# Performance work log

Measured on AMD Instinct MI355X. Metric: run time of the kernel, lower is better.

## Reference

```python
import jax, jax.numpy as jnp
import numpy as np
from jax.scipy.special import logsumexp

B, N, K = 4, 2048, 20          # batch, points per cloud, knn neighbors
D_EMB, H = 512, 4              # embedding dim, attention heads
DH = D_EMB // H                # per-head dim (128)


def setup_inputs() -> dict:
    key = jax.random.key(0)
    ks = jax.random.split(key, 24)
    rn = lambda i, shape, s=0.05: jax.random.normal(ks[i], shape, jnp.float32) * s
    sc = lambda i, c: 1.0 + 0.1 * jax.random.normal(ks[i], (c,), jnp.float32)  # folded BN scale
    return {
        "src": jax.random.normal(ks[0], (B, 3, N), jnp.float32),
        "tgt": jax.random.normal(ks[1], (B, 3, N), jnp.float32),
        # GACLayer (shared for src/tgt): conv(6->64), conv(64->128), out conv(192->512); BN folded to scale/bias
        "g_w1": rn(2, (64, 6)),   "g_s1": sc(3, 64),  "g_b1": rn(4, (64,), 0.02),
        "g_w2": rn(5, (128, 64)), "g_s2": sc(6, 128), "g_b2": rn(7, (128,), 0.02),
        "g_wo": rn(8, (D_EMB, 192)), "g_so": sc(9, D_EMB), "g_bo": rn(10, (D_EMB,), 0.02),
        # MultiHeadedAttention: 3 projection 1x1 convs + merge (all with bias), mlp 1024->512 no bias
        "q_w": rn(11, (D_EMB, D_EMB)), "q_b": rn(12, (D_EMB,), 0.02),
        "k_w": rn(13, (D_EMB, D_EMB)), "k_b": rn(14, (D_EMB,), 0.02),
        "v_w": rn(15, (D_EMB, D_EMB)), "v_b": rn(16, (D_EMB,), 0.02),
        "m_w": rn(17, (D_EMB, D_EMB)), "m_b": rn(18, (D_EMB,), 0.02),
        "mlp_w": rn(19, (D_EMB, 2 * D_EMB)),
    }


def _forward(src, tgt, g_w1, g_s1, g_b1, g_w2, g_s2, g_b2, g_wo, g_so, g_bo,
             q_w, q_b, k_w, k_b, v_w, v_b, m_w, m_b, mlp_w):
    def knn_idx(x):                     # x: [B,3,N] -> [B,N,K] nearest-neighbor indices
        xx = jnp.sum(x * x, axis=1)                      # [B,N]
        inner = jnp.einsum('bdn,bdm->bnm', x, x)
        neg_d = 2.0 * inner - xx[:, :, None] - xx[:, None, :]   # negative sq dist
        return jax.lax.top_k(neg_d, K)[1]                # same as sort-descending[:k]

    def graph_feature(x):               # x: [B,D,N] -> [B,2D,N,K]
        idx = knn_idx(x)
        xt = x.transpose(0, 2, 1)                        # [B,N,D]
        feat = xt[jnp.arange(B)[:, None, None], idx]     # gather: [B,N,K,D]
        ctr = jnp.broadcast_to(xt[:, :, None, :], feat.shape)
        g = jnp.concatenate([feat - ctr, ctr], axis=-1)  # [B,N,K,2D]
        return g.transpose(0, 3, 1, 2)

    def conv_bn_relu2d(w, s, b, x):     # 1x1 conv2d + folded BN (eval) + relu
        y = jnp.einsum('oc,bcnk->bonk', w, x)
        return jax.nn.relu(y * s[:, None, None] + b[:, None, None])

    def attn_pool(h):                   # softmax over neighbors, weighted sum
        a = jax.nn.softmax(h, axis=-1)
        return jnp.sum(h * a, axis=-1)

    def gac(x):                         # GACLayer: [B,3,N] -> [B,512,N]
        g = graph_feature(x)            # [B,6,N,K]
        h1 = conv_bn_relu2d(g_w1, g_s1, g_b1, g)
        x1 = attn_pool(h1)              # [B,64,N]
        h2 = conv_bn_relu2d(g_w2, g_s2, g_b2, h1)
        x2 = attn_pool(h2)              # [B,128,N]
        o = jnp.einsum('oc,bcn->bon', g_wo, jnp.concatenate([x1, x2], axis=1))
        return jax.nn.relu(o * g_so[:, None] + g_bo[:, None])

    def proj(w, b, x):                  # 1x1 conv1d with bias
        return jnp.einsum('oi,bin->bon', w, x) + b[:, None]

    def mha(x, source):                 # note torch view splits channels as (dim, heads)
        q = proj(q_w, q_b, x).reshape(B, DH, H, -1)
        k_ = proj(k_w, k_b, source).reshape(B, DH, H, -1)
        v_ = proj(v_w, v_b, source).reshape(B, DH, H, -1)
        scores = jnp.einsum('bdhn,bdhm->bhnm', q, k_) / jnp.sqrt(jnp.float32(DH))
        prob = jax.nn.softmax(scores, axis=-1)
        msg = jnp.einsum('bhnm,bdhm->bdhn', prob, v_)
        return proj(m_w, m_b, msg.reshape(B, D_EMB, -1))

    def prop(x, source):                # AttentionalPropagation (mlp: 1024->512, no bias/relu)
        msg = mha(x, source)
        return jnp.einsum('oi,bin->bon', mlp_w, jnp.concatenate([x, msg], axis=1))

    def sinkhorn(scores, n_iters=5):    # log-domain Sinkhorn with dustbin row/col (zero pad)
        s = jnp.pad(scores, ((0, 0), (0, 1), (0, 1)))
        for _ in range(n_iters):
            s = jnp.concatenate(
                [s[:, :-1, :] - logsumexp(s[:, :-1, :], axis=2, keepdims=True), s[:, -1:, :]], axis=1)
            s = jnp.concatenate(
                [s[:, :, :-1] - logsumexp(s[:, :, :-1], axis=1, keepdims=True), s[:, :, -1:]], axis=2)
        return s[:, :-1, :-1]

    # embed + cross attentional GNN (shared layer, residual)
    d0, d1 = gac(src), gac(tgt)
    d0, d1 = d0 + prop(d0, d1), d1 + prop(d1, d0)

    dists = jnp.einsum('bdn,bdm->bnm', d0, d1) / jnp.sqrt(jnp.float32(D_EMB))
    perm = jnp.exp(sinkhorn(dists))
    perm_norm = perm / (jnp.sum(perm, axis=2, keepdims=True) + 1e-8)

    weighted_tgt = jnp.einsum('bdm,bnm->bdn', tgt, perm_norm)        # [B,3,N]
    weights = jnp.max(perm, axis=-1, keepdims=True)                  # [B,N,1]
    w_norm = (weights / (jnp.sum(weights, axis=1, keepdims=True) + 1e-8)).transpose(0, 2, 1)  # [B,1,N]
    src_c = jnp.sum(src * w_norm, axis=2, keepdims=True)             # [B,3,1]
    tgt_c = jnp.sum(weighted_tgt * w_norm, axis=2, keepdims=True)
    src_cent = src - src_c
    corr_cent = (weighted_tgt - tgt_c) * w_norm
    Hm = jnp.einsum('bdn,ben->bde', src_cent, corr_cent)             # [B,3,3]

    def solve(Hi):                      # Kabsch with reflection fix (torch.svd returns V, not V^T)
        u, s_, vt = jnp.linalg.svd(Hi)
        v = vt.T
        det = jnp.linalg.det(v @ u.T)
        diag = jnp.diag(jnp.concatenate([jnp.ones(2, Hi.dtype), det[None]]))
        return v @ diag @ u.T

    R = jax.vmap(solve)(Hm)
    t = (-jnp.einsum('bij,bjk->bik', R, src_c) + tgt_c).reshape(B, 3)
    return R, t, perm_norm


def reference(src, tgt, g_w1, g_s1, g_b1, g_w2, g_s2, g_b2, g_wo, g_so, g_bo,
              q_w, q_b, k_w, k_b, v_w, v_b, m_w, m_b, mlp_w):
    return _forward(src, tgt, g_w1, g_s1, g_b1, g_w2, g_s2, g_b2, g_wo, g_so, g_bo,
                    q_w, q_b, k_w, k_b, v_w, v_b, m_w, m_b, mlp_w)
```

## Files before the change

### kernel.cpp

```cpp
#include <hip/hip_runtime.h>
#include <math.h>

#define BATCH 4
#define NP    2048
#define KNNK  20
#define DEMB  512
#define NH    4
#define DHD   128

typedef __attribute__((ext_vector_type(8))) short bf16x8;
typedef __attribute__((ext_vector_type(4))) float f32x4;

__device__ __forceinline__ unsigned short f2b(float f) {
  unsigned u = __builtin_bit_cast(unsigned, f);
  u += 0x7FFF + ((u >> 16) & 1);
  return (unsigned short)(u >> 16);
}
__device__ __forceinline__ float b2f(unsigned short u) {
  unsigned v = ((unsigned)u) << 16;
  return __builtin_bit_cast(float, v);
}

__device__ __forceinline__ void gload_lds16(const void* g, void* l) {
  __builtin_amdgcn_global_load_lds(
// ... 124 lines not shown
    h1f[p][k][o] = y;
    h1b[p * 2048 + k * 64 + (((o >> 3) ^ (k & 7)) << 3) + (o & 7)] = f2b(y);
  }
  __syncthreads();

  {
    int p = w, o = lane;
    float mx = -INFINITY;
#pragma unroll
    for (int k = 0; k < 20; ++k) mx = fmaxf(mx, h1f[p][k][o]);
    float se = 0.f, sh = 0.f;
#pragma unroll
    for (int k = 0; k < 20; ++k) {
      float h = h1f[p][k][o];
      float e = __expf(h - mx);
      se += e; sh += h * e;
    }
    xcg[(size_t)(pbase + p) * 192 + o] = f2b(sh / se);
  }

  bf16x8 bfrag[2][2];
#pragma unroll
  for (int ks = 0; ks < 2; ++ks)
#pragma unroll
    for (int nt = 0; nt < 2; ++nt) {
      int kcol = nt * 16 + lr;
      int oc = ks * 4 + lg;
      bfrag[ks][nt] = *(const bf16x8*)&h1b[w * 2048 + kcol * 64 + ((oc ^ (kcol & 7)) << 3)];
    }
  f32x4 acc[8][2];
#pragma unroll
  for (int i = 0; i < 8; ++i) { acc[i][0] = (f32x4){0,0,0,0}; acc[i][1] = (f32x4){0,0,0,0}; }
#pragma unroll
  for (int i = 0; i < 8; ++i)
#pragma unroll
    for (int ks = 0; ks < 2; ++ks) {
      bf16x8 a = *(const bf16x8*)(w2b + (i * 16 + lr) * 64 + ks * 32 + lg * 8);
      acc[i][0] = __builtin_amdgcn_mfma_f32_16x16x32_bf16(a, bfrag[ks][0], acc[i][0], 0, 0, 0);
      acc[i][1] = __builtin_amdgcn_mfma_f32_16x16x32_bf16(a, bfrag[ks][1], acc[i][1], 0, 0, 0);
    }
  int pt = pbase + w;
#pragma unroll
  for (int i = 0; i < 8; ++i) {
    float x2o[4];
#pragma unroll
    for (int r = 0; r < 4; ++r) {
      int o = i * 16 + lg * 4 + r;
      float sv = s2[o], bv = b2[o];
      float v0 = fmaxf(acc[i][0][r] * sv + bv, 0.f);
      float v1 = fmaxf(acc[i][1][r] * sv + bv, 0.f);
      float vm = (lr < 4) ? fmaxf(v0, v1) : v0;
#pragma unroll
      for (int s = 1; s < 16; s <<= 1) vm = fmaxf(vm, __shfl_xor(vm, s));
      float e0 = __expf(v0 - vm);
      float e1 = (lr < 4) ? __expf(v1 - vm) : 0.f;
      float se = e0 + e1, sh = v0 * e0 + v1 * e1;
#pragma unroll
      for (int s = 1; s < 16; s <<= 1) { se += __shfl_xor(se, s); sh += __shfl_xor(sh, s); }
      x2o[r] = sh / se;
    }
    if (lr == 0) {
      ushort4 pk;
      pk.x = f2b(x2o[0]); pk.y = f2b(x2o[1]); pk.z = f2b(x2o[2]); pk.w = f2b(x2o[3]);
      *(ushort4*)&xcg[(size_t)pt * 192 + 64 + i * 16 + lg * 4] = pk;
    }
  }
}

__global__ __launch_bounds__(256, 2) void gacproj_kernel(
    const unsigned short* __restrict__ wob, const float* __restrict__ so,
    const float* __restrict__ bo, const unsigned short* __restrict__ xcg,
    unsigned short* __restrict__ Y0, unsigned short* __restrict__ Y1) {
  __shared__ __align__(16) unsigned short Al[128 * 64];
  __shared__ __align__(16) unsigned short Bl[128 * 64];
  int n0 = blockIdx.x * 128, o0 = blockIdx.y * 128;
  unsigned short* Yt = (n0 < BATCH * NP) ? Y0 : Y1;
  int nbase = n0 & (BATCH * NP - 1);
  int tid = threadIdx.x, w = tid >> 6, lane = tid & 63;
  int lr = lane & 15, lg = lane >> 4;
  int wa = w >> 1, wb = w & 1;
  f32x4 acc[4][4];
#pragma unroll
  for (int i = 0; i < 4; ++i)
#pragma unroll
    for (int j = 0; j < 4; ++j) acc[i][j] = (f32x4){0.f, 0.f, 0.f, 0.f};

  for (int k0 = 0; k0 < 192; k0 += 64) {
    __syncthreads();
#pragma unroll
    for (int u = 0; u < 4; ++u) {
      int C = u * 256 + tid;
      int row = C >> 3, j = C & 7;
      int js = j ^ (row & 7);
      gload_lds16(wob + (size_t)(o0 + row) * 192 + k0 + js * 8, Al + (u * 256 + w * 64) * 8);
      gload_lds16(xcg + (size_t)(n0 + row) * 192 + k0 + js * 8, Bl + (u * 256 + w * 64) * 8);
    }
    asm volatile("s_waitcnt vmcnt(0)" ::: "memory");
    __syncthreads();
#pragma unroll
    for (int kk = 0; kk < 2; ++kk) {
      bf16x8 af[4], bfr[4];
#pragma unroll
      for (int i = 0; i < 4; ++i) {
        int rowa = wa * 64 + i * 16 + lr;
        int ca = (kk * 4 + lg) ^ (rowa & 7);
        af[i] = *(const bf16x8*)(Al + rowa * 64 + ca * 8);
        int rowb = wb * 64 + i * 16 + lr;
        int cb = (kk * 4 + lg) ^ (rowb & 7);
        bfr[i] = *(const bf16x8*)(Bl + rowb * 64 + cb * 8);
      }
#pragma unroll
      for (int i = 0; i < 4; ++i)
#pragma unroll
        for (int j = 0; j < 4; ++j)
          acc[i][j] = __builtin_amdgcn_mfma_f32_16x16x32_bf16(af[i], bfr[j], acc[i][j], 0, 0, 0);
    }
  }
#pragma unroll
  for (int i = 0; i < 4; ++i) {
#pragma unroll
    for (int j = 0; j < 4; ++j) {
      int obase = o0 + wa * 64 + i * 16 + lg * 4;
      int n = nbase + wb * 64 + j * 16 + lr;
      ushort4 pk;
      pk.x = f2b(fmaxf(acc[i][j][0] * so[obase] + bo[obase], 0.f));
      pk.y = f2b(fmaxf(acc[i][j][1] * so[obase + 1] + bo[obase + 1], 0.f));
      pk.z = f2b(fmaxf(acc[i][j][2] * so[obase + 2] + bo[obase + 2], 0.f));
      pk.w = f2b(fmaxf(acc[i][j][3] * so[obase + 3] + bo[obase + 3], 0.f));
      *(ushort4*)&Yt[(size_t)n * DEMB + obase] = pk;
    }
  }
}

__global__ __launch_bounds__(256, 2) void qkv_kernel(
    const unsigned short* __restrict__ qw, const unsigned short* __restrict__ kw,
    const unsigned short* __restrict__ vw, const float* __restrict__ qbias,
    const float* __restrict__ kbias, const float* __restrict__ vbias,
    const unsigned short* __restrict__ d0t, const unsigned short* __restrict__ d1t,
    unsigned short* __restrict__ Q0, unsigned short* __restrict__ K0,
    unsigned short* __restrict__ V0, unsigned short* __restrict__ Q1,
    unsigned short* __restrict__ K1, unsigned short* __restrict__ V1) {
  __shared__ __align__(16) unsigned short Al[128 * 64];
  __shared__ __align__(16) unsigned short Bl[128 * 64];
  int z = blockIdx.z;
  int b = z & 3, which = z >> 2;
  int proj = which % 3, side = which / 3;
  const unsigned short* Wb = (proj == 0) ? qw : (proj == 1) ? kw : vw;
  const float* bias = (proj == 0) ? qbias : (proj == 1) ? kbias : vbias;
  const unsigned short* Bt = side ? d1t : d0t;
  unsigned short* Y = (which == 0) ? Q0 : (which == 1) ? K0 : (which == 2) ? V0
                    : (which == 3) ? Q1 : (which == 4) ? K1 : V1;
  float pscale = (proj == 0) ? 0.08838834764831845f : 1.f;
  int n0 = blockIdx.x * 128, o0 = blockIdx.y * 128;
  int tid = threadIdx.x, w = tid >> 6, lane = tid & 63;
  int lr = lane & 15, lg = lane >> 4;
  int wa = w >> 1, wb = w & 1;
  f32x4 acc[4][4];
#pragma unroll
  for (int i = 0; i < 4; ++i)
#pragma unroll
    for (int j = 0; j < 4; ++j) acc[i][j] = (f32x4){0.f, 0.f, 0.f, 0.f};

  for (int k0 = 0; k0 < DEMB; k0 += 64) {
    __syncthreads();
#pragma unroll
    for (int u = 0; u < 4; ++u) {
      int C = u * 256 + tid;
      int row = C >> 3, j = C & 7;
      int js = j ^ (row & 7);
      gload_lds16(Wb + (size_t)(o0 + row) * DEMB + k0 + js * 8, Al + (u * 256 + w * 64) * 8);
      gload_lds16(Bt + ((size_t)b * NP + n0 + row) * 512 + k0 + js * 8,
                  Bl + (u * 256 + w * 64) * 8);
    }
    asm volatile("s_waitcnt vmcnt(0)" ::: "memory");
    __syncthreads();
#pragma unroll
    for (int kk = 0; kk < 2; ++kk) {
      bf16x8 af[4], bfr[4];
#pragma unroll
      for (int i = 0; i < 4; ++i) {
        int rowa = wa * 64 + i * 16 + lr;
        int ca = (kk * 4 + lg) ^ (rowa & 7);
        af[i] = *(const bf16x8*)(Al + rowa * 64 + ca * 8);
        int rowb = wb * 64 + i * 16 + lr;
        int cb = (kk * 4 + lg) ^ (rowb & 7);
        bfr[i] = *(const bf16x8*)(Bl + rowb * 64 + cb * 8);
      }
#pragma unroll
      for (int i = 0; i < 4; ++i)
#pragma unroll
        for (int j = 0; j < 4; ++j)
          acc[i][j] = __builtin_amdgcn_mfma_f32_16x16x32_bf16(af[i], bfr[j], acc[i][j], 0, 0, 0);
    }
  }
#pragma unroll
  for (int i = 0; i < 4; ++i) {
#pragma unroll
    for (int j = 0; j < 4; ++j) {
#pragma unroll
      for (int r = 0; r < 4; ++r) {
        int o = o0 + wa * 64 + i * 16 + lg * 4 + r;
        int n = n0 + wb * 64 + j * 16 + lr;
        float v = (acc[i][j][r] + bias[o]) * pscale;
        int h = o & 3, dh = o >> 2;
        if (proj < 2) {
          Y[(((size_t)b * NH + h) * NP + n) * DHD + dh] = f2b(v);
        } else {
          Y[(((size_t)b * NH + h) * DHD + dh) * NP + n] = f2b(v);
        }
      }
    }
  }
}

template <int MODE, int KD>
__global__ __launch_bounds__(256, 2) void proj_mfma_kernel(
    const unsigned short* __restrict__ Wb, const float* __restrict__ bias,
    const unsigned short* __restrict__ Bt0, const unsigned short* __restrict__ Bt1,
    const unsigned short* __restrict__ Bt2_0, const unsigned short* __restrict__ Bt2_1,
    const unsigned short* __restrict__ D0, const unsigned short* __restrict__ D1,
    unsigned short* __restrict__ Y0, unsigned short* __restrict__ Y1) {
  __shared__ __align__(16) unsigned short Al[128 * 64];
  __shared__ __align__(16) unsigned short Bl[128 * 64];
  int z = blockIdx.z;
  int b = z & 3, side = z >> 2;
  const unsigned short* Bt = side ? Bt1 : Bt0;
  const unsigned short* Bt2 = side ? Bt2_1 : Bt2_0;
  const unsigned short* Dres = side ? D1 : D0;
  unsigned short* Y = side ? Y1 : Y0;
  int n0 = blockIdx.x * 128, o0 = blockIdx.y * 128;
  int tid = threadIdx.x, w = tid >> 6, lane = tid & 63;
  int lr = lane & 15, lg = lane >> 4;
  int wa = w >> 1, wb = w & 1;
  f32x4 acc[4][4];
#pragma unroll
  for (int i = 0; i < 4; ++i)
#pragma unroll
    for (int j = 0; j < 4; ++j) acc[i][j] = (f32x4){0.f, 0.f, 0.f, 0.f};

  for (int k0 = 0; k0 < KD; k0 += 64) {
    __syncthreads();
    const unsigned short* srcB; int kc;
    if (MODE == 4) { srcB = (k0 < 512) ? Bt : Bt2; kc = k0 & 511; }
    else { srcB = Bt; kc = k0; }
#pragma unroll
    for (int u = 0; u < 4; ++u) {
      int C = u * 256 + tid;
      int row = C >> 3, j = C & 7;
      int js = j ^ (row & 7);
      gload_lds16(Wb + (size_t)(o0 + row) * KD + k0 + js * 8, Al + (u * 256 + w * 64) * 8);
      gload_lds16(srcB + ((size_t)b * NP + n0 + row) * 512 + kc + js * 8,
                  Bl + (u * 256 + w * 64) * 8);
    }
    asm volatile("s_waitcnt vmcnt(0)" ::: "memory");
    __syncthreads();
#pragma unroll
    for (int kk = 0; kk < 2; ++kk) {
      bf16x8 af[4], bfr[4];
#pragma unroll
      for (int i = 0; i < 4; ++i) {
        int rowa = wa * 64 + i * 16 + lr;
        int ca = (kk * 4 + lg) ^ (rowa & 7);
        af[i] = *(const bf16x8*)(Al + rowa * 64 + ca * 8);
        int rowb = wb * 64 + i * 16 + lr;
        int cb = (kk * 4 + lg) ^ (rowb & 7);
        bfr[i] = *(const bf16x8*)(Bl + rowb * 64 + cb * 8);
      }
#pragma unroll
      for (int i = 0; i < 4; ++i)
#pragma unroll
        for (int j = 0; j < 4; ++j)
          acc[i][j] = __builtin_amdgcn_mfma_f32_16x16x32_bf16(af[i], bfr[j], acc[i][j], 0, 0, 0);
    }
  }
#pragma unroll
  for (int i = 0; i < 4; ++i) {
#pragma unroll
    for (int j = 0; j < 4; ++j) {
#pragma unroll
      for (int r = 0; r < 4; ++r) {
        int o = o0 + wa * 64 + i * 16 + lg * 4 + r;
        int n = n0 + wb * 64 + j * 16 + lr;
        float v = acc[i][j][r];
        if (MODE == 3) {
          v += bias[o];
        } else {
          v += b2f(Dres[((size_t)b * NP + n) * DEMB + o]);
        }
        Y[((size_t)b * NP + n) * DEMB + o] = f2b(v);
      }
    }
  }
}

__global__ __launch_bounds__(256, 2) void attn_mfma_kernel(
    const unsigned short* __restrict__ Q0, const unsigned short* __restrict__ K0,
    const unsigned short* __restrict__ V0, const unsigned short* __restrict__ Q1,
    const unsigned short* __restrict__ K1, const unsigned short* __restrict__ V1,
    unsigned short* __restrict__ att0, unsigned short* __restrict__ att1) {
  __shared__ __align__(16) unsigned short Klds[2][8192];
  __shared__ __align__(16) unsigned short Vlds[2][8192];
  __shared__ __align__(16) float Pws[4][544];

  int which = blockIdx.x >> 9;
  int blk = blockIdx.x & 511;
  const unsigned short* Qb = which ? Q1 : Q0;
  const unsigned short* Kb = which ? K0 : K1;
  const unsigned short* Vb = which ? V0 : V1;
  unsigned short* att = which ? att1 : att0;

  int bh = blk >> 5, qt = blk & 31;
  int tid = threadIdx.x;
  int w = tid >> 6, lane = tid & 63;
  int lr = lane & 15, lg = lane >> 4;
  int q0 = qt * 64 + w * 16;

  const unsigned short* Qrow = Qb + ((size_t)bh * NP + q0 + lr) * DHD + lg * 8;
  bf16x8 qf[4];
#pragma unroll
  for (int ds = 0; ds < 4; ++ds) qf[ds] = *(const bf16x8*)(Qrow + ds * 32);

  const unsigned short* Kg = Kb + (size_t)bh * NP * DHD;
  const unsigned short* Vg = Vb + (size_t)bh * DHD * NP;
  unsigned short* Pl = (unsigned short*)&Pws[w][0];

  f32x4 o[8];
#pragma unroll
  for (int ds = 0; ds < 8; ++ds) o[ds] = (f32x4){0.f, 0.f, 0.f, 0.f};
  float mrun[4] = {-INFINITY, -INFINITY, -INFINITY, -INFINITY};
  float lrun[4] = {0.f, 0.f, 0.f, 0.f};

#pragma unroll
  for (int u = 0; u < 4; ++u) {
    int C = (w * 4 + u) * 64 + lane;
    int key = C >> 4, jl = C & 15, j = jl ^ (key & 15);
    gload_lds16(Kg + (size_t)key * DHD + j * 8, &Klds[0][(w * 4 + u) * 512]);
    int d = C >> 3, jv = (C & 7) ^ (d & 7);
    gload_lds16(Vg + (size_t)d * NP + jv * 8, &Vlds[0][(w * 4 + u) * 512]);
  }
  asm volatile("s_waitcnt vmcnt(0)" ::: "memory");
  __syncthreads();

  for (int tIdx = 0; tIdx < 32; ++tIdx) {
    int cur = tIdx & 1;
    if (tIdx < 31) {
      int kv0 = (tIdx + 1) * 64;
#pragma unroll
      for (int u = 0; u < 4; ++u) {
        int C = (w * 4 + u) * 64 + lane;
        int key = C >> 4, jl = C & 15, j = jl ^ (key & 15);
        gload_lds16(Kg + (size_t)(kv0 + key) * DHD + j * 8, &Klds[cur ^ 1][(w * 4 + u) * 512]);
        int d = C >> 3, jv = (C & 7) ^ (d & 7);
        gload_lds16(Vg + (size_t)d * NP + kv0 + jv * 8, &Vlds[cur ^ 1][(w * 4 + u) * 512]);
      }
    }
    f32x4 s[4];
#pragma unroll
    for (int ks = 0; ks < 4; ++ks) {
      s[ks] = (f32x4){0.f, 0.f, 0.f, 0.f};
      int key = ks * 16 + lr;
#pragma unroll
      for (int dstep = 0; dstep < 4; ++dstep) {
        int dbyte = (lg * 16 + dstep * 64) ^ ((key & 15) << 4);
        bf16x8 kb = *(const bf16x8*)(&Klds[cur][0] + key * 128 + (dbyte >> 1));
        s[ks] = __builtin_amdgcn_mfma_f32_16x16x32_bf16(qf[dstep], kb, s[ks], 0, 0, 0);
      }
    }
    float tmax[4];
#pragma unroll
    for (int r = 0; r < 4; ++r) {
      float m = fmaxf(fmaxf(s[0][r], s[1][r]), fmaxf(s[2][r], s[3][r]));
#pragma unroll
      for (int msk = 1; msk < 16; msk <<= 1) m = fmaxf(m, __shfl_xor(m, msk));
      tmax[r] = m;
    }
    int need = 0;
#pragma unroll
    for (int r = 0; r < 4; ++r) need |= (tmax[r] > mrun[r]) ? 1 : 0;
    float fac[4] = {1.f, 1.f, 1.f, 1.f};
    if (__any(need)) {
#pragma unroll
      for (int r = 0; r < 4; ++r) {
        float mnew = fmaxf(mrun[r], tmax[r]);
        fac[r] = __expf(mrun[r] - mnew);
        mrun[r] = mnew;
      }
#pragma unroll
      for (int ds = 0; ds < 8; ++ds)
#pragma unroll
        for (int r = 0; r < 4; ++r) o[ds][r] *= fac[r];
    }
    float ps[4] = {0.f, 0.f, 0.f, 0.f};
#pragma unroll
    for (int ks = 0; ks < 4; ++ks) {
      int k = ks * 16 + lr;
#pragma unroll
      for (int r = 0; r < 4; ++r) {
        float p = __expf(s[ks][r] - mrun[r]);
        ps[r] += p;
        int q = lg * 4 + r;
        int kbyte = (k * 2) ^ ((q & 7) << 4);
        Pl[q * 64 + (kbyte >> 1)] = f2b(p);
      }
    }
#pragma unroll
    for (int r = 0; r < 4; ++r) {
#pragma unroll
      for (int msk = 1; msk < 16; msk <<= 1) ps[r] += __shfl_xor(ps[r], msk);
      lrun[r] = lrun[r] * fac[r] + ps[r];
    }
#pragma unroll
    for (int ks2 = 0; ks2 < 2; ++ks2) {
      int kbyte = ((lg * 8 + ks2 * 32) * 2) ^ ((lr & 7) << 4);
      bf16x8 pa = *(const bf16x8*)(Pl + lr * 64 + (kbyte >> 1));
#pragma unroll
      for (int ds = 0; ds < 8; ++ds) {
        int d = ds * 16 + lr;
        int keybyte = ((lg * 8 + ks2 * 32) * 2) ^ ((d & 7) << 4);
        bf16x8 vb = *(const bf16x8*)(&Vlds[cur][0] + d * 64 + (keybyte >> 1));
        o[ds] = __builtin_amdgcn_mfma_f32_16x16x32_bf16(pa, vb, o[ds], 0, 0, 0);
      }
    }
    asm volatile("s_waitcnt vmcnt(0)" ::: "memory");
    __syncthreads();
  }

  float linv[4];
#pragma unroll
  for (int r = 0; r < 4; ++r) linv[r] = 1.f / lrun[r];
  float* ost = &Pws[w][0];
  int b = bh >> 2, h = bh & 3;
  unsigned short* outb = att + ((size_t)b * NP + q0) * DEMB;
#pragma unroll
  for (int c = 0; c < 4; ++c) {
#pragma unroll
    for (int half = 0; half < 2; ++half) {
      int ds = 2 * c + half;
#pragma unroll
      for (int r = 0; r < 4; ++r)
        ost[(lg * 4 + r) * 33 + half * 16 + lr] = o[ds][r] * linv[r];
    }
#pragma unroll
    for (int it = 0; it < 8; ++it) {
      int q = lr, dl = it * 4 + lg;
      int d = c * 32 + dl;
      outb[(size_t)q * DEMB + d * 4 + h] = f2b(ost[q * 33 + dl]);
    }
  }
}

__global__ __launch_bounds__(256, 2) void dists_mfma_kernel(
    const unsigned short* __restrict__ At, const unsigned short* __restrict__ Bt,
    unsigned short* __restrict__ S) {
  __shared__ __align__(16) unsigned short Sh[2][8192];
  int b = blockIdx.z;
  int n0 = blockIdx.y * 128, m0 = blockIdx.x * 128;
  int tid = threadIdx.x, w = tid >> 6, lane = tid & 63;
  int lr = lane & 15, lg = lane >> 4;
  int wn = w >> 1, wm = w & 1;
  const unsigned short* Ab = At + ((size_t)b * NP + n0) * DEMB;
  const unsigned short* Bb = Bt + ((size_t)b * NP + m0) * DEMB;
  f32x4 acc[4][4];
#pragma unroll
  for (int i = 0; i < 4; ++i)
#pragma unroll
    for (int j = 0; j < 4; ++j) acc[i][j] = (f32x4){0.f, 0.f, 0.f, 0.f};

  for (int k0 = 0; k0 < DEMB; k0 += 64) {
    __syncthreads();
#pragma unroll
    for (int u = 0; u < 4; ++u) {
      int C = u * 256 + tid;
      int row = C >> 3, j = C & 7;
      int js = j ^ (row & 7);
      gload_lds16(Ab + (size_t)row * DEMB + k0 + js * 8, &Sh[0][(u * 256 + w * 64) * 8]);
      gload_lds16(Bb + (size_t)row * DEMB + k0 + js * 8, &Sh[1][(u * 256 + w * 64) * 8]);
    }
    asm volatile("s_waitcnt vmcnt(0)" ::: "memory");
    __syncthreads();
#pragma unroll
    for (int kk = 0; kk < 2; ++kk) {
      bf16x8 af[4], bfr[4];
#pragma unroll
      for (int i = 0; i < 4; ++i) {
        int rowa = wn * 64 + i * 16 + lr;
        int ca = (kk * 4 + lg) ^ (rowa & 7);
        af[i] = *(const bf16x8*)(&Sh[0][0] + rowa * 64 + ca * 8);
        int rowb = wm * 64 + i * 16 + lr;
        int cb = (kk * 4 + lg) ^ (rowb & 7);
        bfr[i] = *(const bf16x8*)(&Sh[1][0] + rowb * 64 + cb * 8);
      }
#pragma unroll
      for (int i = 0; i < 4; ++i)
#pragma unroll
        for (int j = 0; j < 4; ++j)
          acc[i][j] = __builtin_amdgcn_mfma_f32_16x16x32_bf16(af[i], bfr[j], acc[i][j], 0, 0, 0);
    }
  }
  const float scale = 0.04419417382415922f;
  __syncthreads();
  unsigned short* Cs = &Sh[0][0];
#pragma unroll
  for (int i = 0; i < 4; ++i)
#pragma unroll
    for (int j = 0; j < 4; ++j)
#pragma unroll
      for (int r = 0; r < 4; ++r) {
        int nl = wn * 64 + i * 16 + lg * 4 + r;
        int ml = wm * 64 + j * 16 + lr;
        Cs[nl * 128 + ml] = f2b(acc[i][j][r] * scale);
      }
  __syncthreads();
  unsigned short* Sb = S + (size_t)b * NP * NP;
#pragma unroll
  for (int it = 0; it < 8; ++it) {
    int chunk = it * 256 + tid;
    int rowl = chunk >> 4, c8 = (chunk & 15) * 8;
    *(bf16x8*)(Sb + (size_t)(n0 + rowl) * NP + m0 + c8) = *(const bf16x8*)(Cs + rowl * 128 + c8);
  }
}

__global__ __launch_bounds__(256) void sink_u_kernel(const unsigned short* __restrict__ S,
                                                     const float* __restrict__ v,
                                                     float* __restrict__ u) {
  int t = threadIdx.x, w = t >> 6, lane = t & 63;
  int rowid = blockIdx.x * 4 + w;
  int b = rowid >> 11, i = rowid & 2047;
  const unsigned short* row = S + ((size_t)b * NP + i) * NP;
  const float* vb = v + (size_t)b * NP;
  float m = -INFINITY, s = 0.f;
#pragma unroll
  for (int c = 0; c < 4; ++c) {
    int off = c * 512 + lane * 8;
    bf16x8 x8 = *(const bf16x8*)(row + off);
    float4 va = *(const float4*)(vb + off);
    float4 vc = *(const float4*)(vb + off + 4);
    float xs[8];
    xs[0] = b2f(x8[0]) + va.x; xs[1] = b2f(x8[1]) + va.y;
    xs[2] = b2f(x8[2]) + va.z; xs[3] = b2f(x8[3]) + va.w;
    xs[4] = b2f(x8[4]) + vc.x; xs[5] = b2f(x8[5]) + vc.y;
    xs[6] = b2f(x8[6]) + vc.z; xs[7] = b2f(x8[7]) + vc.w;
    float mc = fmaxf(fmaxf(fmaxf(xs[0], xs[1]), fmaxf(xs[2], xs[3])),
                     fmaxf(fmaxf(xs[4], xs[5]), fmaxf(xs[6], xs[7])));
    float sc = 0.f;
#pragma unroll
    for (int e = 0; e < 8; ++e) sc += __expf(xs[e] - mc);
    float M = fmaxf(m, mc);
    s = s * __expf(m - M) + sc * __expf(mc - M);
    m = M;
  }
#pragma unroll
  for (int st = 1; st < 64; st <<= 1) {
    float m2 = __shfl_xor(m, st), s2 = __shfl_xor(s, st);
    float M = fmaxf(m, m2);
    s = s * __expf(m - M) + s2 * __expf(m2 - M);
    m = M;
  }
  if (lane == 0) {
    float M = fmaxf(m, 0.f);
    float ss = s * __expf(m - M) + __expf(-M);
    u[(size_t)b * NP + i] = -(M + logf(ss));
  }
}

__global__ void sink_c1_kernel(const unsigned short* __restrict__ S, const float* __restrict__ u,
                               float* __restrict__ colM, float* __restrict__ colS) {
  int ctile = blockIdx.x, part = blockIdx.y, b = blockIdx.z;
  int t = threadIdx.x, ry = t >> 6, cx = t & 63;
  int c0 = ctile * 128 + cx * 2;
  int rbase = part * 256 + ry * 64;
  const unsigned short* Sb = S + (size_t)b * NP * NP;
  const float* ub = u + (size_t)b * NP;
  float m0 = -INFINITY, s0 = 0.f, m1 = -INFINITY, s1 = 0.f;
  for (int r8 = 0; r8 < 64; r8 += 8) {
    float x0[8], x1[8];
#pragma unroll
    for (int k = 0; k < 8; ++k) {
      int r = rbase + r8 + k;
      unsigned pk = *(const unsigned*)(Sb + (size_t)r * NP + c0);
      float uu = ub[r];
      x0[k] = b2f((unsigned short)pk) + uu;
      x1[k] = b2f((unsigned short)(pk >> 16)) + uu;
    }
    float mc0 = x0[0], mc1 = x1[0];
#pragma unroll
    for (int k = 1; k < 8; ++k) { mc0 = fmaxf(mc0, x0[k]); mc1 = fmaxf(mc1, x1[k]); }
    float sc0 = 0.f, sc1 = 0.f;
#pragma unroll
    for (int k = 0; k < 8; ++k) { sc0 += __expf(x0[k] - mc0); sc1 += __expf(x1[k] - mc1); }
    float M0 = fmaxf(m0, mc0);
    s0 = s0 * __expf(m0 - M0) + sc0 * __expf(mc0 - M0); m0 = M0;
    float M1 = fmaxf(m1, mc1);
    s1 = s1 * __expf(m1 - M1) + sc1 * __expf(mc1 - M1); m1 = M1;
  }
  __shared__ float pm[4][128], ps[4][128];
  pm[ry][cx * 2] = m0; pm[ry][cx * 2 + 1] = m1;
  ps[ry][cx * 2] = s0; ps[ry][cx * 2 + 1] = s1;
  __syncthreads();
  if (t < 128) {
    float m = pm[0][t], s = ps[0][t];
    for (int k = 1; k < 4; ++k) {
      float m2 = pm[k][t], s2 = ps[k][t];
      float M = fmaxf(m, m2);
      s = s * __expf(m - M) + s2 * __expf(m2 - M);
      m = M;
    }
    size_t oo = ((size_t)b * NP + ctile * 128 + t) * 8 + part;
    colM[oo] = m; colS[oo] = s;
  }
}

__global__ void sink_c2_kernel(const float* __restrict__ colM, const float* __restrict__ colS,
                               float* __restrict__ v) {
  int i = blockIdx.x * 256 + threadIdx.x;
  if (i >= BATCH * NP) return;
  float m = -INFINITY, s = 0.f;
  for (int p = 0; p < 8; ++p) {
    float m2 = colM[(size_t)i * 8 + p], s2 = colS[(size_t)i * 8 + p];
    float M = fmaxf(m, m2);
    s = s * __expf(m - M) + s2 * __expf(m2 - M);
    m = M;
  }
  float M = fmaxf(m, 0.f);
  s = s * __expf(m - M) + __expf(-M);
  v[i] = -(M + logf(s));
}

__global__ void perm_kernel(const unsigned short* __restrict__ S, const float* __restrict__ u,
                            const float* __restrict__ v, const float* __restrict__ tgt,
                            float* __restrict__ outp, float* __restrict__ weights,
                            float* __restrict__ wt) {
  int b = blockIdx.x / NP, n = blockIdx.x % NP, t = threadIdx.x;
  const unsigned short* row = S + ((size_t)b * NP + n) * NP;
  const float* vb = v + (size_t)b * NP;
  float ui = u[(size_t)b * NP + n];
  __shared__ float reds[256], redm[256];
  int c0 = t * 8;
  bf16x8 x8 = *(const bf16x8*)(row + c0);
  float4 va = *(const float4*)(vb + c0);
  float4 vc = *(const float4*)(vb + c0 + 4);
  float ev[8];
  ev[0] = __expf(b2f(x8[0]) + ui + va.x); ev[1] = __expf(b2f(x8[1]) + ui + va.y);
  ev[2] = __expf(b2f(x8[2]) + ui + va.z); ev[3] = __expf(b2f(x8[3]) + ui + va.w);
  ev[4] = __expf(b2f(x8[4]) + ui + vc.x); ev[5] = __expf(b2f(x8[5]) + ui + vc.y);
  ev[6] = __expf(b2f(x8[6]) + ui + vc.z); ev[7] = __expf(b2f(x8[7]) + ui + vc.w);
  float lsum = 0.f, lm = -INFINITY;
#pragma unroll
  for (int e = 0; e < 8; ++e) { lsum += ev[e]; lm = fmaxf(lm, ev[e]); }
  reds[t] = lsum; redm[t] = lm;
  __syncthreads();
  for (int st = 128; st > 0; st >>= 1) {
    if (t < st) { reds[t] += reds[t + st]; redm[t] = fmaxf(redm[t], redm[t + st]); }
    __syncthreads();
  }
  float inv = 1.f / (reds[0] + 1e-8f);
  float mx = redm[0];
  __syncthreads();
  const float* tb = tgt + (size_t)b * 3 * NP;
  float* op = outp + ((size_t)b * NP + n) * NP;
  float pn[8];
#pragma unroll
  for (int e = 0; e < 8; ++e) pn[e] = ev[e] * inv;
  float4 o0 = {pn[0], pn[1], pn[2], pn[3]};
  float4 o1 = {pn[4], pn[5], pn[6], pn[7]};
  *(float4*)(op + c0) = o0;
  *(float4*)(op + c0 + 4) = o1;
  float av[3];
#pragma unroll
  for (int d = 0; d < 3; ++d) {
    const float* td = tb + d * NP;
    float4 ta = *(const float4*)(td + c0);
    float4 tc = *(const float4*)(td + c0 + 4);
    av[d] = pn[0] * ta.x + pn[1] * ta.y + pn[2] * ta.z + pn[3] * ta.w +
            pn[4] * tc.x + pn[5] * tc.y + pn[6] * tc.z + pn[7] * tc.w;
  }
  for (int d = 0; d < 3; ++d) {
    reds[t] = av[d];
    __syncthreads();
    for (int st = 128; st > 0; st >>= 1) { if (t < st) reds[t] += reds[t + st]; __syncthreads(); }
    if (t == 0) wt[((size_t)b * 3 + d) * NP + n] = reds[0];
    __syncthreads();
  }
  if (t == 0) weights[(size_t)b * NP + n] = mx;
}

__global__ void wsum_kernel(const float* __restrict__ weights, float* __restrict__ wsum) {
  int b = blockIdx.x, t = threadIdx.x;
  __shared__ float red[256];
  float s = 0.f;
  for (int n = t; n < NP; n += 256) s += weights[(size_t)b * NP + n];
  red[t] = s;
  __syncthreads();
  for (int st = 128; st > 0; st >>= 1) { if (t < st) red[t] += red[t + st]; __syncthreads(); }
  if (t == 0) wsum[b] = red[0];
}

__global__ void cent_hm_kernel(const float* __restrict__ src, const float* __restrict__ wt,
                               const float* __restrict__ weights, const float* __restrict__ wsum,
                               float* __restrict__ cent, float* __restrict__ Hm) {
  int b = blockIdx.x, t = threadIdx.x;
  __shared__ float red[256];
  __shared__ float cc[6];
  float inv = 1.f / (wsum[b] + 1e-8f);
  const float* sb = src + (size_t)b * 3 * NP;
  const float* wb = wt + (size_t)b * 3 * NP;
  const float* ww = weights + (size_t)b * NP;
  float acc[6] = {};
  for (int n = t; n < NP; n += 256) {
    float w = ww[n] * inv;
    acc[0] += sb[n] * w;        acc[1] += sb[NP + n] * w;  acc[2] += sb[2 * NP + n] * w;
    acc[3] += wb[n] * w;        acc[4] += wb[NP + n] * w;  acc[5] += wb[2 * NP + n] * w;
  }
  for (int i = 0; i < 6; ++i) {
    red[t] = acc[i];
    __syncthreads();
    for (int st = 128; st > 0; st >>= 1) { if (t < st) red[t] += red[t + st]; __syncthreads(); }
    if (t == 0) cc[i] = red[0];
    __syncthreads();
  }
  float h[9] = {};
  for (int n = t; n < NP; n += 256) {
    float w = ww[n] * inv;
    float s0 = sb[n] - cc[0], s1 = sb[NP + n] - cc[1], s2 = sb[2 * NP + n] - cc[2];
    float d0 = (wb[n] - cc[3]) * w, d1 = (wb[NP + n] - cc[4]) * w, d2 = (wb[2 * NP + n] - cc[5]) * w;
    h[0] += s0 * d0; h[1] += s0 * d1; h[2] += s0 * d2;
    h[3] += s1 * d0; h[4] += s1 * d1; h[5] += s1 * d2;
    h[6] += s2 * d0; h[7] += s2 * d1; h[8] += s2 * d2;
  }
  for (int i = 0; i < 9; ++i) {
    red[t] = h[i];
    __syncthreads();
    for (int st = 128; st > 0; st >>= 1) { if (t < st) red[t] += red[t + st]; __syncthreads(); }
    if (t == 0) Hm[b * 9 + i] = red[0];
    __syncthreads();
  }
  if (t == 0) for (int i = 0; i < 6; ++i) cent[b * 6 + i] = cc[i];
}

__device__ double det3d(const double M[3][3]) {
  return M[0][0] * (M[1][1] * M[2][2] - M[1][2] * M[2][1])
       - M[0][1] * (M[1][0] * M[2][2] - M[1][2] * M[2][0])
       + M[0][2] * (M[1][0] * M[2][1] - M[1][1] * M[2][0]);
}

#define JROT(p, q)                                                              \
  do {                                                                          \
    double apq = S[p][q];                                                       \
    if (fabs(apq) > 1e-60) {                                                    \
      double tau = (S[q][q] - S[p][p]) / (2.0 * apq);                           \
      double tt = (tau >= 0.0) ? 1.0 / (tau + sqrt(1.0 + tau * tau))            \
                               : 1.0 / (tau - sqrt(1.0 + tau * tau));           \
      double cr = 1.0 / sqrt(1.0 + tt * tt), sr = tt * cr;                      \
      _Pragma("unroll") for (int k = 0; k < 3; ++k) {                           \
        double skp = S[k][p], skq = S[k][q];                                    \
        S[k][p] = cr * skp - sr * skq;  S[k][q] = sr * skp + cr * skq;          \
      }                                                                         \
      _Pragma("unroll") for (int k = 0; k < 3; ++k) {                           \
        double spk = S[p][k], sqk = S[q][k];                                    \
        S[p][k] = cr * spk - sr * sqk;  S[q][k] = sr * spk + cr * sqk;          \
      }                                                                         \
      _Pragma("unroll") for (int k = 0; k < 3; ++k) {                           \
        double vkp = V[k][p], vkq = V[k][q];                                    \
        V[k][p] = cr * vkp - sr * vkq;  V[k][q] = sr * vkp + cr * vkq;          \
      }                                                                         \
    }                                                                           \
  } while (0)

#define CSWAPCOL(i, j, ei, ej)                                                  \
  if (ei < ej) {                                                                \
    double tt_ = ei; ei = ej; ej = tt_;                                         \
    _Pragma("unroll") for (int r = 0; r < 3; ++r) {                             \
      double tv = V[r][i]; V[r][i] = V[r][j]; V[r][j] = tv;                     \
    }                                                                           \
  }

__global__ void solve_kernel(const float* __restrict__ Hm, const float* __restrict__ cent,
                             float* __restrict__ out) {
  int b = threadIdx.x;
  if (b >= BATCH) return;
  double A[3][3];
#pragma unroll
  for (int r = 0; r < 3; ++r)
#pragma unroll
    for (int c = 0; c < 3; ++c) A[r][c] = (double)Hm[b * 9 + r * 3 + c];
  double S[3][3];
#pragma unroll
  for (int i = 0; i < 3; ++i)
#pragma unroll
    for (int j = 0; j < 3; ++j) {
      double acc = 0.0;
#pragma unroll
      for (int k = 0; k < 3; ++k) acc += A[k][i] * A[k][j];
      S[i][j] = acc;
    }
  double V[3][3] = {{1, 0, 0}, {0, 1, 0}, {0, 0, 1}};
  for (int sweep = 0; sweep < 12; ++sweep) {
    JROT(0, 1); JROT(0, 2); JROT(1, 2);
  }
  double e0 = S[0][0], e1 = S[1][1], e2 = S[2][2];
  CSWAPCOL(0, 1, e0, e1);
  CSWAPCOL(0, 2, e0, e2);
  CSWAPCOL(1, 2, e1, e2);
  double Us[3][3];
#pragma unroll
  for (int i = 0; i < 3; ++i) {
    double v0 = V[0][i], v1 = V[1][i], v2 = V[2][i];
    double u0 = A[0][0] * v0 + A[0][1] * v1 + A[0][2] * v2;
    double u1 = A[1][0] * v0 + A[1][1] * v1 + A[1][2] * v2;
    double u2 = A[2][0] * v0 + A[2][1] * v1 + A[2][2] * v2;
    double nrm = sqrt(u0 * u0 + u1 * u1 + u2 * u2);
    if (nrm > 1e-30) { u0 /= nrm; u1 /= nrm; u2 /= nrm; }
    else if (i == 2) {
      u0 = Us[1][0] * Us[2][1] - Us[2][0] * Us[1][1];
      u1 = Us[2][0] * Us[0][1] - Us[0][0] * Us[2][1];
      u2 = Us[0][0] * Us[1][1] - Us[1][0] * Us[0][1];
      double nn = sqrt(u0 * u0 + u1 * u1 + u2 * u2);
      if (nn > 1e-30) { u0 /= nn; u1 /= nn; u2 /= nn; }
    }
    Us[0][i] = u0; Us[1][i] = u1; Us[2][i] = u2;
  }
  double d = det3d(V) * det3d(Us);
  double R[3][3];
#pragma unroll
  for (int i = 0; i < 3; ++i)
#pragma unroll
    for (int j = 0; j < 3; ++j)
      R[i][j] = V[i][0] * Us[j][0] + V[i][1] * Us[j][1] + d * V[i][2] * Us[j][2];
  double sc[3] = {(double)cent[b * 6 + 0], (double)cent[b * 6 + 1], (double)cent[b * 6 + 2]};
  double tc[3] = {(double)cent[b * 6 + 3], (double)cent[b * 6 + 4], (double)cent[b * 6 + 5]};
#pragma unroll
  for (int r = 0; r < 3; ++r)
#pragma unroll
    for (int c = 0; c < 3; ++c) out[b * 9 + r * 3 + c] = (float)R[r][c];
#pragma unroll
  for (int i = 0; i < 3; ++i) {
    double tv = tc[i] - (R[i][0] * sc[0] + R[i][1] * sc[1] + R[i][2] * sc[2]);
    out[36 + b * 3 + i] = (float)tv;
  }
}

extern "C" void kernel_launch(void* const* d_in, const int* in_sizes, int n_in,
                              void* d_out, int out_size, void* d_ws, size_t ws_size,
                              hipStream_t stream) {
  const float* src  = (const float*)d_in[0];
  const float* tgt  = (const float*)d_in[1];
  const float* g_w1 = (const float*)d_in[2];
  const float* g_s1 = (const float*)d_in[3];
  const float* g_b1 = (const float*)d_in[4];
  const float* g_w2 = (const float*)d_in[5];
  const float* g_s2 = (const float*)d_in[6];
  const float* g_b2 = (const float*)d_in[7];
  const float* g_wo = (const float*)d_in[8];
  const float* g_so = (const float*)d_in[9];
  const float* g_bo = (const float*)d_in[10];
  const float* q_w  = (const float*)d_in[11];
  const float* q_b  = (const float*)d_in[12];
  const float* k_w  = (const float*)d_in[13];
  const float* k_b  = (const float*)d_in[14];
  const float* v_w  = (const float*)d_in[15];
  const float* v_b  = (const float*)d_in[16];
  const float* m_w  = (const float*)d_in[17];
  const float* m_b  = (const float*)d_in[18];
  const float* mlp_w = (const float*)d_in[19];
  float* out = (float*)d_out;
  float* ws = (float*)d_ws;

  const size_t SLOT = 4194304;
  unsigned short* d0t  = (unsigned short*)(ws + 0 * SLOT);
  unsigned short* d1t  = (unsigned short*)(ws + 1 * SLOT);
  unsigned short* Q0   = (unsigned short*)(ws + 2 * SLOT);
  unsigned short* K0   = (unsigned short*)(ws + 3 * SLOT);
  unsigned short* V0   = (unsigned short*)(ws + 4 * SLOT);
  unsigned short* Q1   = (unsigned short*)(ws + 5 * SLOT);
  unsigned short* K1   = (unsigned short*)(ws + 6 * SLOT);
  unsigned short* V1   = (unsigned short*)(ws + 7 * SLOT);
  unsigned short* att0t = (unsigned short*)(ws + 8 * SLOT);
  unsigned short* att1t = (unsigned short*)(ws + 9 * SLOT);
  unsigned short* mp0t = Q0;
  unsigned short* mp1t = Q1;
  unsigned short* d0nt = att0t;
  unsigned short* d1nt = att1t;
  unsigned short* base3  = (unsigned short*)(ws + 3 * SLOT);
  unsigned short* q_wb   = base3 + 4456448;
  unsigned short* k_wb   = q_wb + 262144;
  unsigned short* v_wb   = k_wb + 262144;
  unsigned short* m_wb   = v_wb + 262144;
  unsigned short* mlp_wb = m_wb + 262144;
  unsigned short* w2b    = mlp_wb + 524288;
  unsigned short* wob    = w2b + 8192;
  unsigned short* xcg    = att0t;
  unsigned short* SbU = (unsigned short*)ws;
  int*   idx0 = (int*)(ws + 10 * SLOT);
  int*   idx1 = idx0 + BATCH * NP * KNNK;
  float* colM = ws + 10 * SLOT + 327680;
  float* colS = colM + BATCH * NP * 8;
  float* weights = colS + BATCH * NP * 8;
  float* wsum = weights + BATCH * NP;
  float* wtg  = wsum + BATCH;
  float* cent = wtg + BATCH * 3 * NP;
  float* Hmb  = cent + BATCH * 6;
  float* upot = Hmb + BATCH * 9;
  float* vpot = upot + BATCH * NP;

  conv_all_kernel<<<1648, 256, 0, stream>>>(q_w, k_w, v_w, m_w, mlp_w, g_w2, g_wo,
                                            q_wb, k_wb, v_wb, m_wb, mlp_wb, w2b, wob, vpot);
  knn2_kernel<<<2 * BATCH * NP / 4, 256, 0, stream>>>(src, tgt, idx0, idx1);
  gac4_kernel<<<2 * BATCH * NP / 4, 256, 0, stream>>>(src, tgt, idx0, idx1, g_w1, g_s1, g_b1,
                                                      w2b, g_s2, g_b2, xcg);
  dim3 gg(2 * BATCH * NP / 128, DEMB / 128);
  gacproj_kernel<<<gg, 256, 0, stream>>>(wob, g_so, g_bo, xcg, d0t, d1t);
  dim3 gqkv(NP / 128, DEMB / 128, 24);
  qkv_kernel<<<gqkv, 256, 0, stream>>>(q_wb, k_wb, v_wb, q_b, k_b, v_b, d0t, d1t,
                                       Q0, K0, V0, Q1, K1, V1);
  attn_mfma_kernel<<<2 * 16 * 32, 256, 0, stream>>>(Q0, K0, V0, Q1, K1, V1, att0t, att1t);
  dim3 gq8(NP / 128, DEMB / 128, 8);
  proj_mfma_kernel<3, 512><<<gq8, 256, 0, stream>>>(m_wb, m_b, att0t, att1t, nullptr, nullptr,
                                                    nullptr, nullptr, mp0t, mp1t);
  proj_mfma_kernel<4, 1024><<<gq8, 256, 0, stream>>>(mlp_wb, nullptr, d0t, d1t, mp0t, mp1t,
                                                     d0t, d1t, d0nt, d1nt);
  dists_mfma_kernel<<<dim3(NP / 128, NP / 128, BATCH), 256, 0, stream>>>(d0nt, d1nt, SbU);
  for (int it = 0; it < 5; ++it) {
    sink_u_kernel<<<BATCH * NP / 4, 256, 0, stream>>>(SbU, vpot, upot);
    sink_c1_kernel<<<dim3(NP / 128, 8, BATCH), 256, 0, stream>>>(SbU, upot, colM, colS);
    sink_c2_kernel<<<(BATCH * NP + 255) / 256, 256, 0, stream>>>(colM, colS, vpot);
  }
  perm_kernel<<<BATCH * NP, 256, 0, stream>>>(SbU, upot, vpot, tgt, out + 48, weights, wtg);
  wsum_kernel<<<BATCH, 256, 0, stream>>>(weights, wsum);
  cent_hm_kernel<<<BATCH, 256, 0, stream>>>(src, wtg, weights, wsum, cent, Hmb);
  solve_kernel<<<1, 64, 0, stream>>>(Hmb, cent, out);
}
```

Baseline: 682.5 us.

## Process two 16-query fragments per wave in attention to reuse K/V tiles

Each wave in the attention kernel now handles 32 query rows as two 16-row MFMA fragments instead of 16, so each block covers 128 queries and the grid is halved. Every K/V tile loaded into LDS, and each K fragment read from it, is now used by twice as many queries, cutting global K/V traffic and LDS reads per unit of work. In exchange, accumulator and score register use per thread roughly doubles, and the smaller grid exposes fewer blocks for latency hiding. The shared per-wave P scratch buffer is reused in turn by the two fragments.

```diff
diff --git a/kernel.cpp b/kernel.cpp
--- a/kernel.cpp
+++ b/kernel.cpp
@@ -450,33 +450,41 @@
   __shared__ __align__(16) unsigned short Vlds[2][8192];
   __shared__ __align__(16) float Pws[4][544];
 
-  int which = blockIdx.x >> 9;
-  int blk = blockIdx.x & 511;
+  int which = blockIdx.x >> 8;
+  int blk = blockIdx.x & 255;
   const unsigned short* Qb = which ? Q1 : Q0;
   const unsigned short* Kb = which ? K0 : K1;
   const unsigned short* Vb = which ? V0 : V1;
   unsigned short* att = which ? att1 : att0;
 
-  int bh = blk >> 5, qt = blk & 31;
+  int bh = blk >> 4, qt = blk & 15;
   int tid = threadIdx.x;
   int w = tid >> 6, lane = tid & 63;
   int lr = lane & 15, lg = lane >> 4;
-  int q0 = qt * 64 + w * 16;
-
-  const unsigned short* Qrow = Qb + ((size_t)bh * NP + q0 + lr) * DHD + lg * 8;
-  bf16x8 qf[4];
-#pragma unroll
-  for (int ds = 0; ds < 4; ++ds) qf[ds] = *(const bf16x8*)(Qrow + ds * 32);
+  int q0 = qt * 128 + w * 32;
+
+  bf16x8 qf[2][4];
+#pragma unroll
+  for (int f = 0; f < 2; ++f) {
+    const unsigned short* Qrow = Qb + ((size_t)bh * NP + q0 + f * 16 + lr) * DHD + lg * 8;
+#pragma unroll
+    for (int ds = 0; ds < 4; ++ds) qf[f][ds] = *(const bf16x8*)(Qrow + ds * 32);
+  }
 
   const unsigned short* Kg = Kb + (size_t)bh * NP * DHD;
   const unsigned short* Vg = Vb + (size_t)bh * DHD * NP;
   unsigned short* Pl = (unsigned short*)&Pws[w][0];
 
-  f32x4 o[8];
-#pragma unroll
-  for (int ds = 0; ds < 8; ++ds) o[ds] = (f32x4){0.f, 0.f, 0.f, 0.f};
-  float mrun[4] = {-INFINITY, -INFINITY, -INFINITY, -INFINITY};
-  float lrun[4] = {0.f, 0.f, 0.f, 0.f};
+  f32x4 o[2][8];
+#pragma unroll
+  for (int f = 0; f < 2; ++f)
+#pragma unroll
+    for (int ds = 0; ds < 8; ++ds) o[f][ds] = (f32x4){0.f, 0.f, 0.f, 0.f};
+  float mrun[2][4], lrun[2][4];
+#pragma unroll
+  for (int f = 0; f < 2; ++f)
+#pragma unroll
+    for (int r = 0; r < 4; ++r) { mrun[f][r] = -INFINITY; lrun[f][r] = 0.f; }
 
 #pragma unroll
   for (int u = 0; u < 4; ++u) {
@@ -502,97 +510,117 @@
         gload_lds16(Vg + (size_t)d * NP + kv0 + jv * 8, &Vlds[cur ^ 1][(w * 4 + u) * 512]);
       }
     }
-    f32x4 s[4];
+    f32x4 s[2][4];
 #pragma unroll
     for (int ks = 0; ks < 4; ++ks) {
-      s[ks] = (f32x4){0.f, 0.f, 0.f, 0.f};
+      s[0][ks] = (f32x4){0.f, 0.f, 0.f, 0.f};
+      s[1][ks] = (f32x4){0.f, 0.f, 0.f, 0.f};
       int key = ks * 16 + lr;
 #pragma unroll
       for (int dstep = 0; dstep < 4; ++dstep) {
         int dbyte = (lg * 16 + dstep * 64) ^ ((key & 15) << 4);
         bf16x8 kb = *(const bf16x8*)(&Klds[cur][0] + key * 128 + (dbyte >> 1));
-        s[ks] = __builtin_amdgcn_mfma_f32_16x16x32_bf16(qf[dstep], kb, s[ks], 0, 0, 0);
-      }
-    }
-    float tmax[4];
-#pragma unroll
-    for (int r = 0; r < 4; ++r) {
-      float m = fmaxf(fmaxf(s[0][r], s[1][r]), fmaxf(s[2][r], s[3][r]));
-#pragma unroll
-      for (int msk = 1; msk < 16; msk <<= 1) m = fmaxf(m, __shfl_xor(m, msk));
-      tmax[r] = m;
-    }
+        s[0][ks] = __builtin_amdgcn_mfma_f32_16x16x32_bf16(qf[0][dstep], kb, s[0][ks], 0, 0, 0);
+        s[1][ks] = __builtin_amdgcn_mfma_f32_16x16x32_bf16(qf[1][dstep], kb, s[1][ks], 0, 0, 0);
+      }
+    }
+    float tmax[2][4];
+#pragma unroll
+    for (int f = 0; f < 2; ++f)
+#pragma unroll
+      for (int r = 0; r < 4; ++r) {
+        float m = fmaxf(fmaxf(s[f][0][r], s[f][1][r]), fmaxf(s[f][2][r], s[f][3][r]));
+#pragma unroll
+        for (int msk = 1; msk < 16; msk <<= 1) m = fmaxf(m, __shfl_xor(m, msk));
+        tmax[f][r] = m;
+      }
     int need = 0;
 #pragma unroll
-    for (int r = 0; r < 4; ++r) need |= (tmax[r] > mrun[r]) ? 1 : 0;
-    float fac[4] = {1.f, 1.f, 1.f, 1.f};
+    for (int f = 0; f < 2; ++f)
+#pragma unroll
+      for (int r = 0; r < 4; ++r) need |= (tmax[f][r] > mrun[f][r]) ? 1 : 0;
+    float fac[2][4];
+#pragma unroll
+    for (int f = 0; f < 2; ++f)
+#pragma unroll
+      for (int r = 0; r < 4; ++r) fac[f][r] = 1.f;
     if (__any(need)) {
 #pragma unroll
+      for (int f = 0; f < 2; ++f)
+#pragma unroll
+        for (int r = 0; r < 4; ++r) {
+          float mnew = fmaxf(mrun[f][r], tmax[f][r]);
+          fac[f][r] = __expf(mrun[f][r] - mnew);
+          mrun[f][r] = mnew;
+        }
+#pragma unroll
+      for (int f = 0; f < 2; ++f)
+#pragma unroll
+        for (int ds = 0; ds < 8; ++ds)
+#pragma unroll
+          for (int r = 0; r < 4; ++r) o[f][ds][r] *= fac[f][r];
+    }
+#pragma unroll
+    for (int f = 0; f < 2; ++f) {
+      float ps[4] = {0.f, 0.f, 0.f, 0.f};
+#pragma unroll
+      for (int ks = 0; ks < 4; ++ks) {
+        int k = ks * 16 + lr;
+#pragma unroll
+        for (int r = 0; r < 4; ++r) {
+          float p = __expf(s[f][ks][r] - mrun[f][r]);
+          ps[r] += p;
+          int q = lg * 4 + r;
+          int kbyte = (k * 2) ^ ((q & 7) << 4);
+          Pl[q * 64 + (kbyte >> 1)] = f2b(p);
+        }
+      }
+#pragma unroll
       for (int r = 0; r < 4; ++r) {
-        float mnew = fmaxf(mrun[r], tmax[r]);
-        fac[r] = __expf(mrun[r] - mnew);
-        mrun[r] = mnew;
-      }
-#pragma unroll
-      for (int ds = 0; ds < 8; ++ds)
-#pragma unroll
-        for (int r = 0; r < 4; ++r) o[ds][r] *= fac[r];
-    }
-    float ps[4] = {0.f, 0.f, 0.f, 0.f};
-#pragma unroll
-    for (int ks = 0; ks < 4; ++ks) {
-      int k = ks * 16 + lr;
-#pragma unroll
-      for (int r = 0; r < 4; ++r) {
-        float p = __expf(s[ks][r] - mrun[r]);
-        ps[r] += p;
-        int q = lg * 4 + r;
-        int kbyte = (k * 2) ^ ((q & 7) << 4);
-        Pl[q * 64 + (kbyte >> 1)] = f2b(p);
-      }
-    }
-#pragma unroll
-    for (int r = 0; r < 4; ++r) {
-#pragma unroll
-      for (int msk = 1; msk < 16; msk <<= 1) ps[r] += __shfl_xor(ps[r], msk);
-      lrun[r] = lrun[r] * fac[r] + ps[r];
-    }
-#pragma unroll
-    for (int ks2 = 0; ks2 < 2; ++ks2) {
-      int kbyte = ((lg * 8 + ks2 * 32) * 2) ^ ((lr & 7) << 4);
-      bf16x8 pa = *(const bf16x8*)(Pl + lr * 64 + (kbyte >> 1));
-#pragma unroll
-      for (int ds = 0; ds < 8; ++ds) {
-        int d = ds * 16 + lr;
-        int keybyte = ((lg * 8 + ks2 * 32) * 2) ^ ((d & 7) << 4);
-        bf16x8 vb = *(const bf16x8*)(&Vlds[cur][0] + d * 64 + (keybyte >> 1));
-        o[ds] = __builtin_amdgcn_mfma_f32_16x16x32_bf16(pa, vb, o[ds], 0, 0, 0);
+#pragma unroll
+        for (int msk = 1; msk < 16; msk <<= 1) ps[r] += __shfl_xor(ps[r], msk);
+        lrun[f][r] = lrun[f][r] * fac[f][r] + ps[r];
+      }
+#pragma unroll
+      for (int ks2 = 0; ks2 < 2; ++ks2) {
+        int kbyte = ((lg * 8 + ks2 * 32) * 2) ^ ((lr & 7) << 4);
+        bf16x8 pa = *(const bf16x8*)(Pl + lr * 64 + (kbyte >> 1));
+#pragma unroll
+        for (int ds = 0; ds < 8; ++ds) {
+          int d = ds * 16 + lr;
+          int keybyte = ((lg * 8 + ks2 * 32) * 2) ^ ((d & 7) << 4);
+          bf16x8 vb = *(const bf16x8*)(&Vlds[cur][0] + d * 64 + (keybyte >> 1));
+          o[f][ds] = __builtin_amdgcn_mfma_f32_16x16x32_bf16(pa, vb, o[f][ds], 0, 0, 0);
+        }
       }
     }
     asm volatile("s_waitcnt vmcnt(0)" ::: "memory");
     __syncthreads();
   }
 
-  float linv[4];
-#pragma unroll
-  for (int r = 0; r < 4; ++r) linv[r] = 1.f / lrun[r];
+  int b = bh >> 2, h = bh & 3;
   float* ost = &Pws[w][0];
-  int b = bh >> 2, h = bh & 3;
-  unsigned short* outb = att + ((size_t)b * NP + q0) * DEMB;
-#pragma unroll
-  for (int c = 0; c < 4; ++c) {
-#pragma unroll
-    for (int half = 0; half < 2; ++half) {
-      int ds = 2 * c + half;
-#pragma unroll
-      for (int r = 0; r < 4; ++r)
-        ost[(lg * 4 + r) * 33 + half * 16 + lr] = o[ds][r] * linv[r];
-    }
-#pragma unroll
-    for (int it = 0; it < 8; ++it) {
-      int q = lr, dl = it * 4 + lg;
-      int d = c * 32 + dl;
-      outb[(size_t)q * DEMB + d * 4 + h] = f2b(ost[q * 33 + dl]);
+#pragma unroll
+  for (int f = 0; f < 2; ++f) {
+    float linv[4];
+#pragma unroll
+    for (int r = 0; r < 4; ++r) linv[r] = 1.f / lrun[f][r];
+    unsigned short* outb = att + ((size_t)b * NP + q0 + f * 16) * DEMB;
+#pragma unroll
+    for (int c = 0; c < 4; ++c) {
+#pragma unroll
+      for (int half = 0; half < 2; ++half) {
+        int ds = 2 * c + half;
+#pragma unroll
+        for (int r = 0; r < 4; ++r)
+          ost[(lg * 4 + r) * 33 + half * 16 + lr] = o[f][ds][r] * linv[r];
+      }
+#pragma unroll
+      for (int it = 0; it < 8; ++it) {
+        int q = lr, dl = it * 4 + lg;
+        int d = c * 32 + dl;
+        outb[(size_t)q * DEMB + d * 4 + h] = f2b(ost[q * 33 + dl]);
+      }
     }
   }
 }
@@ -1060,7 +1088,7 @@
   dim3 gqkv(NP / 128, DEMB / 128, 24);
   qkv_kernel<<<gqkv, 256, 0, stream>>>(q_wb, k_wb, v_wb, q_b, k_b, v_b, d0t, d1t,
                                        Q0, K0, V0, Q1, K1, V1);
-  attn_mfma_kernel<<<2 * 16 * 32, 256, 0, stream>>>(Q0, K0, V0, Q1, K1, V1, att0t, att1t);
+  attn_mfma_kernel<<<2 * 16 * 16, 256, 0, stream>>>(Q0, K0, V0, Q1, K1, V1, att0t, att1t);
   dim3 gq8(NP / 128, DEMB / 128, 8);
   proj_mfma_kernel<3, 512><<<gq8, 256, 0, stream>>>(m_wb, m_b, att0t, att1t, nullptr, nullptr,
                                                     nullptr, nullptr, mp0t, mp1t);
```

After: 657.2 us. 1.04x faster.
